# Optimization experiments

Hardware: AMD Instinct MI355X
Metric: run time of the kernel (lower is better)

The kernel has to match this reference:

```python
import jax, jax.numpy as jnp
import numpy as np

N = 50000   # nodes
E = 800000  # edges (before self-loops)
B = 256     # graphs in batch
F = 128     # input feature dim
H = 4       # heads per layer
C = 64      # out_channels per head
NEG_SLOPE = 0.2


def setup_inputs() -> dict:
    key = jax.random.key(0)
    ks = jax.random.split(key, 16)
    s = 0.05
    inp = {
        "x": jax.random.normal(ks[0], (N, F), dtype=jnp.float32),
        "edge_index": jax.random.randint(ks[1], (2, E), 0, N, dtype=jnp.int32),
        "batch": jnp.sort(jax.random.randint(ks[2], (N,), 0, B, dtype=jnp.int32)),
        # layer 1: F -> H*C
        "W1": jax.random.normal(ks[3], (F, H * C), dtype=jnp.float32) * s,
        "as1": jax.random.normal(ks[4], (H, C), dtype=jnp.float32) * s,
        "ad1": jax.random.normal(ks[5], (H, C), dtype=jnp.float32) * s,
        "b1": jnp.zeros((H * C,), dtype=jnp.float32),
        # layer 2: H*C -> H*C
        "W2": jax.random.normal(ks[6], (H * C, H * C), dtype=jnp.float32) * s,
        "as2": jax.random.normal(ks[7], (H, C), dtype=jnp.float32) * s,
        "ad2": jax.random.normal(ks[8], (H, C), dtype=jnp.float32) * s,
        "b2": jnp.zeros((H * C,), dtype=jnp.float32),
        # layer 3: H*C -> H*C
        "W3": jax.random.normal(ks[9], (H * C, H * C), dtype=jnp.float32) * s,
        "as3": jax.random.normal(ks[10], (H, C), dtype=jnp.float32) * s,
        "ad3": jax.random.normal(ks[11], (H, C), dtype=jnp.float32) * s,
        "b3": jnp.zeros((H * C,), dtype=jnp.float32),
    }
    return inp


def _gat_layer(x, src, dst, W, a_src, a_dst, bias):
    """PyG GATConv (concat=True, self-loops already included in src/dst)."""
    n = x.shape[0]
    xh = (x @ W).reshape(n, H, C)                      # [N,H,C]
    alpha_s = jnp.sum(xh * a_src, axis=-1)             # [N,H]
    alpha_d = jnp.sum(xh * a_dst, axis=-1)             # [N,H]
    logits = alpha_s[src] + alpha_d[dst]               # [E',H]
    logits = jnp.where(logits > 0, logits, NEG_SLOPE * logits)  # LeakyReLU
    # segment-wise softmax over destination neighborhoods
    m = jax.lax.stop_gradient(jax.ops.segment_max(logits, dst, num_segments=n))
    e = jnp.exp(logits - m[dst])
    z = jax.ops.segment_sum(e, dst, num_segments=n)
    alpha = e / (z[dst] + 1e-16)                       # [E',H]
    msg = xh[src] * alpha[:, :, None]                  # [E',H,C]
    out = jax.ops.segment_sum(msg, dst, num_segments=n)  # [N,H,C]
    return out.reshape(n, H * C) + bias


def reference(x, edge_index, batch, W1, as1, ad1, b1, W2, as2, ad2, b2, W3, as3, ad3, b3):
    n = x.shape[0]
    loops = jnp.arange(n, dtype=edge_index.dtype)
    src = jnp.concatenate([edge_index[0], loops])
    dst = jnp.concatenate([edge_index[1], loops])
    # dropout is identity at inference; activation = ReLU between layers
    h = jax.nn.relu(_gat_layer(x, src, dst, W1, as1, ad1, b1))
    h = jax.nn.relu(_gat_layer(h, src, dst, W2, as2, ad2, b2))
    h = _gat_layer(h, src, dst, W3, as3, ad3, b3)
    pooled = jax.ops.segment_max(h, batch, num_segments=B)  # global max pool -> [B, H*C]
    return jnp.squeeze(pooled)
```

## Files before the change

kernel.cpp:

```cpp
#include <hip/hip_runtime.h>
#include <hip/hip_fp16.h>
#include <math.h>

#define NN 50000
#define NE 800000
#define NT 850000
#define NB 256
#define FIN 128
#define HC 256
#define NH 4
#define CD 64
#define NEG 0.2f
#define SCAN_B 196
#define PSPL 8

typedef _Float16 half8 __attribute__((ext_vector_type(8)));
typedef float f32x4 __attribute__((ext_vector_type(4)));

__device__ __forceinline__ void gld16(const void* g, void* l) {
    __builtin_amdgcn_global_load_lds(
        (const __attribute__((address_space(1))) void*)g,
        (__attribute__((address_space(3))) void*)l, 16, 0, 0);
}


__global__ void zero_int_kernel(int* __restrict__ p, int n) {
    int i = blockIdx.x * blockDim.x + threadIdx.x;
    if (i < n) p[i] = 0;
}

__global__ void hist_kernel(const int* __restrict__ ei, int* __restrict__ cnt) {
    int e = blockIdx.x * blockDim.x + threadIdx.x;
    if (e < NE) {
        atomicAdd(&cnt[ei[NE + e]], 1);
    } else if (e < NT) {
        atomicAdd(&cnt[e - NE], 1);
    }
}

__global__ __launch_bounds__(256) void part_kernel(const int* __restrict__ cnt,
                                                   int* __restrict__ part) {
    __shared__ int red[4];
    int i = blockIdx.x * 256 + threadIdx.x;
    int v = (i < NN) ? cnt[i] : 0;
#pragma unroll
    for (int off = 32; off > 0; off >>= 1) v += __shfl_down(v, off);
    if ((threadIdx.x & 63) == 0) red[threadIdx.x >> 6] = v;
    __syncthreads();
    if (threadIdx.x == 0) part[blockIdx.x] = red[0] + red[1] + red[2] + red[3];
}

__global__ __launch_bounds__(256) void offs_kernel(const int* __restrict__ part,
                                                   int* __restrict__ boff) {
    __shared__ int sh[256];
    int t = threadIdx.x;
    sh[t] = (t < SCAN_B) ? part[t] : 0;
    __syncthreads();
    for (int off = 1; off < 256; off <<= 1) {
        int add = (t >= off) ? sh[t - off] : 0;
        __syncthreads();
        sh[t] += add;
        __syncthreads();
    }
    boff[t] = (t == 0) ? 0 : sh[t - 1];
}

__global__ __launch_bounds__(256) void write_scan_kernel(const int* __restrict__ cnt,
        const int* __restrict__ boff, int* __restrict__ rowptr, int* __restrict__ cursor) {
    __shared__ int sh[256];
    int t = threadIdx.x;
    int i = blockIdx.x * 256 + t;
    int v = (i < NN) ? cnt[i] : 0;
    sh[t] = v;
    __syncthreads();
    for (int off = 1; off < 256; off <<= 1) {
        int add = (t >= off) ? sh[t - off] : 0;
        __syncthreads();
        sh[t] += add;
        __syncthreads();
    }
    int run = boff[blockIdx.x] + sh[t] - v;
    if (i < NN) { rowptr[i] = run; cursor[i] = run; }
    if (i == NN - 1) rowptr[NN] = run + v;
}

__global__ void scatter_kernel(const int* __restrict__ ei, int* __restrict__ cursor,
                               int* __restrict__ colsrc) {
    int e = blockIdx.x * blockDim.x + threadIdx.x;
    int s, d;
    if (e < NE)      { s = ei[e]; d = ei[NE + e]; }
    else if (e < NT) { s = e - NE; d = s; }
    else return;
    int pos = atomicAdd(&cursor[d], 1);
    colsrc[pos] = s;
}

__global__ void batch_bounds_kernel(const int* __restrict__ batch, int* __restrict__ bstart) {
    int i = blockIdx.x * blockDim.x + threadIdx.x;
    if (i >= NN) return;
    int b = batch[i];
    if (i == 0) {
        for (int bb = 0; bb <= b; ++bb) bstart[bb] = 0;
    } else {
        int pb = batch[i - 1];
        if (pb != b) for (int bb = pb + 1; bb <= b; ++bb) bstart[bb] = i;
    }
    if (i == NN - 1) {
        for (int bb = b + 1; bb <= NB; ++bb) bstart[bb] = NN;
    }
}


template<int K>
__global__ __launch_bounds__(256) void wprep_kernel(const float* __restrict__ W,
                                                    _Float16* __restrict__ WtS) {
    __shared__ float sm[8][257];
    const int t = threadIdx.x;
    const int kb = blockIdx.x * 8;
#pragma unroll
    for (int i = 0; i < 8; ++i) {
        int idx = i * 256 + t;
        sm[idx >> 8][idx & 255] = W[(size_t)(kb + (idx >> 8)) * HC + (idx & 255)];
    }
    __syncthreads();
    half8 o;
#pragma unroll
    for (int r = 0; r < 8; ++r) o[r] = (_Float16)sm[r][t];
    *reinterpret_cast<half8*>(&WtS[((size_t)blockIdx.x * 256 + t) * 8]) = o;
}


template<int K, bool F32IN>
__global__ __launch_bounds__(256) void mfma_gemm_kernel(
        const _Float16* __restrict__ Xh, const _Float16* __restrict__ Xl,
        const float* __restrict__ Xf,
        const _Float16* __restrict__ WtS, __half* __restrict__ XHo,
        const float* __restrict__ as_g, const float* __restrict__ ad_g,
        float* __restrict__ aS, float* __restrict__ aD) {
    constexpr int C2 = 2 * K;
    constexpr int NSTEP = C2 / 32;
    constexpr int SPP = K / 32;
    __shared__ __align__(16) _Float16 As[4][64 * 32];
    __shared__ __align__(16) _Float16 Bs[4][32 * 128];
    const int t = threadIdx.x;
    const int lane = t & 63;
    const int wid = t >> 6;
    const int wm = wid & 1, wn = wid >> 1;
    const int cbb = blockIdx.x & 1;
    const int r0 = (blockIdx.x >> 1) * 64;
    const int cb0 = cbb * 128;
    const int l15 = lane & 15;
    const int kcl = lane >> 4;
    const int srowA = t >> 2;
    const int skcA  = t & 3;
    const int arow = min(r0 + srowA, NN - 1);

    f32x4 acc[2][4];
#pragma unroll
    for (int i = 0; i < 2; ++i)
#pragma unroll
        for (int j = 0; j < 4; ++j) acc[i][j] = (f32x4)0.f;

    float4 rA[3][2];

    auto loadA = [&](int s, float4& v0, float4& v1) {
        const int cbase = (s % SPP) * 32;
        if constexpr (F32IN) {
            const float* p = Xf + (size_t)arow * K + cbase + skcA * 8;
            v0 = *reinterpret_cast<const float4*>(p);
            v1 = *reinterpret_cast<const float4*>(p + 4);
        } else {
            const _Float16* src = (s < SPP) ? Xh : Xl;
            v0 = *reinterpret_cast<const float4*>(src + (size_t)arow * K + cbase + skcA * 8);
        }
    };
    auto writeA = [&](int s, int buf, float4 v0, float4 v1) {
        _Float16* d = &As[buf][(skcA * 64 + (srowA ^ skcA)) * 8];
        if constexpr (F32IN) {
            float f[8];
            *reinterpret_cast<float4*>(f) = v0;
            *reinterpret_cast<float4*>(f + 4) = v1;
            half8 h;
#pragma unroll
            for (int e = 0; e < 8; ++e) {
                _Float16 a = (_Float16)f[e];
                h[e] = (s >= SPP) ? (_Float16)(f[e] - (float)a) : a;
            }
            *reinterpret_cast<half8*>(d) = h;
        } else {
            *reinterpret_cast<float4*>(d) = v0;
        }
    };
    auto issueB = [&](int s, int buf) {
        const int kbase = (s % SPP) * 4;
#pragma unroll
        for (int r2 = 0; r2 < 2; ++r2) {
            int kc = r2 * 2 + (t >> 7);
            int col = t & 127;
            gld16(WtS + ((size_t)(kbase + kc) * 256 + cb0 + col) * 8,
                  &Bs[buf][(kc * 128 + col) * 8]);
        }
    };
    auto mfma_step = [&](int s, int buf) {
        half8 a0 = *reinterpret_cast<const half8*>(
            &As[buf][(kcl * 64 + ((wm * 32      + l15) ^ kcl)) * 8]);
        half8 a1 = *reinterpret_cast<const half8*>(
            &As[buf][(kcl * 64 + ((wm * 32 + 16 + l15) ^ kcl)) * 8]);
        const _Float16* bp = &Bs[buf][(kcl * 128 + wn * 64 + l15) * 8];
        __builtin_amdgcn_s_setprio(1);
#pragma unroll
        for (int nf = 0; nf < 4; ++nf) {
            half8 b = *reinterpret_cast<const half8*>(bp + nf * 16 * 8);
            acc[0][nf] = __builtin_amdgcn_mfma_f32_16x16x32_f16(a0, b, acc[0][nf], 0, 0, 0);
            acc[1][nf] = __builtin_amdgcn_mfma_f32_16x16x32_f16(a1, b, acc[1][nf], 0, 0, 0);
        }
        __builtin_amdgcn_s_setprio(0);
    };
    auto wait_steady = [&]() {
        if constexpr (F32IN) asm volatile("s_waitcnt vmcnt(8) lgkmcnt(0)" ::: "memory");
        else                 asm volatile("s_waitcnt vmcnt(6) lgkmcnt(0)" ::: "memory");
        __builtin_amdgcn_s_barrier();
        __builtin_amdgcn_sched_barrier(0);
    };

    loadA(0, rA[0][0], rA[0][1]); issueB(0, 0);
    loadA(1, rA[1][0], rA[1][1]); issueB(1, 1);
    loadA(2, rA[2][0], rA[2][1]); issueB(2, 2);
    writeA(0, 0, rA[0][0], rA[0][1]);
    wait_steady();

#pragma unroll
    for (int s = 0; s < NSTEP - 3; ++s) {
        loadA(s + 3, rA[(s + 3) % 3][0], rA[(s + 3) % 3][1]);
        issueB(s + 3, (s + 3) & 3);
        mfma_step(s, s & 3);
        writeA(s + 1, (s + 1) & 3, rA[(s + 1) % 3][0], rA[(s + 1) % 3][1]);
        wait_steady();
    }
    mfma_step(NSTEP - 3, (NSTEP - 3) & 3);
    writeA(NSTEP - 2, (NSTEP - 2) & 3, rA[(NSTEP - 2) % 3][0], rA[(NSTEP - 2) % 3][1]);
    if constexpr (F32IN) asm volatile("s_waitcnt vmcnt(4) lgkmcnt(0)" ::: "memory");
    else                 asm volatile("s_waitcnt vmcnt(3) lgkmcnt(0)" ::: "memory");
    __builtin_amdgcn_s_barrier();
    __builtin_amdgcn_sched_barrier(0);
    mfma_step(NSTEP - 2, (NSTEP - 2) & 3);
    writeA(NSTEP - 1, (NSTEP - 1) & 3, rA[(NSTEP - 1) % 3][0], rA[(NSTEP - 1) % 3][1]);
    asm volatile("s_waitcnt vmcnt(0) lgkmcnt(0)" ::: "memory");
    __builtin_amdgcn_s_barrier();
    __builtin_amdgcn_sched_barrier(0);
    mfma_step(NSTEP - 1, (NSTEP - 1) & 3);

    const int rb = r0 + wm * 32 + (lane >> 4) * 4;
    const int cbg = cb0 + wn * 64 + l15;
    const int head = cbb * 2 + wn;
    float asv[4], adv[4];
#pragma unroll
    for (int nf = 0; nf < 4; ++nf) {
        asv[nf] = as_g[cbg + nf * 16];
        adv[nf] = ad_g[cbg + nf * 16];
    }
#pragma unroll
    for (int mf = 0; mf < 2; ++mf)
#pragma unroll
        for (int r = 0; r < 4; ++r) {
            int row = rb + mf * 16 + r;
            float s0 = 0.f, d0 = 0.f;
#pragma unroll
            for (int nf = 0; nf < 4; ++nf) {
                float a = acc[mf][nf][r];
                s0 += a * asv[nf];
                d0 += a * adv[nf];
            }
#pragma unroll
            for (int off = 1; off < 16; off <<= 1) {
                s0 += __shfl_xor(s0, off);
                d0 += __shfl_xor(d0, off);
            }
            if (row < NN) {
                if (l15 == 0) {
                    aS[row * 4 + head] = s0;
                    aD[row * 4 + head] = d0;
                }
#pragma unroll
                for (int nf = 0; nf < 4; ++nf)
                    XHo[(size_t)row * HC + cbg + nf * 16] = __float2half(acc[mf][nf][r]);
            }
        }
}


#define LEAKY(v) ((v) > 0.f ? (v) : NEG * (v))

template<int RELU, int SPLIT>
__global__ __launch_bounds__(256) void aggregate_kernel(
        const int* __restrict__ rowptr, const int* __restrict__ colsrc,
        const float* __restrict__ aS, const float* __restrict__ aD,
        const __half* __restrict__ XH,
        const float* __restrict__ bias, float* __restrict__ OUT,
        __half* __restrict__ OUTh, __half* __restrict__ OUTl) {
    __shared__ float4 wbuf[4][64];
    __shared__ int    ibuf[4][64];
    const int wslot = threadIdx.x >> 6;
    int n = blockIdx.x * 4 + wslot;
    int lane = threadIdx.x & 63;
    bool lo = lane < 32;
    const __half2* xbase = reinterpret_cast<const __half2*>(XH);
    float4 adv = *reinterpret_cast<const float4*>(aD + n * 4);
    float zl = 0.f, zh = 0.f;
    float al0 = 0.f, al1 = 0.f, ah0 = 0.f, ah1 = 0.f;
    int jb = rowptr[n], je = rowptr[n + 1];
    for (int c0 = jb; c0 < je; c0 += 64) {
        int cnt = min(64, je - c0);
        {
            int e = min(c0 + lane, je - 1);
            int s = colsrc[e];
            float4 sv = *reinterpret_cast<const float4*>(aS + s * 4);
            float4 w;
            w.x = __expf(LEAKY(sv.x + adv.x));
            w.y = __expf(LEAKY(sv.y + adv.y));
            w.z = __expf(LEAKY(sv.z + adv.z));
            w.w = __expf(LEAKY(sv.w + adv.w));
            wbuf[wslot][lane] = w;
            ibuf[wslot][lane] = s;
        }
        int u = 0;
        for (; u + 8 <= cnt; u += 8) {
            int sidx[8];
            float4 w[8];
#pragma unroll
            for (int k = 0; k < 8; ++k) { sidx[k] = ibuf[wslot][u + k]; w[k] = wbuf[wslot][u + k]; }
            __half2 p[8], q[8];
#pragma unroll
            for (int k = 0; k < 8; ++k) {
                const __half2* xp = xbase + (size_t)sidx[k] * (HC / 2) + lane;
                p[k] = xp[0];
                q[k] = xp[64];
            }
#pragma unroll
            for (int k = 0; k < 8; ++k) {
                float wl = lo ? w[k].x : w[k].y, wh = lo ? w[k].z : w[k].w;
                float2 f = __half22float2(p[k]);
                al0 += wl * f.x; al1 += wl * f.y;
                f = __half22float2(q[k]);
                ah0 += wh * f.x; ah1 += wh * f.y;
                zl += wl; zh += wh;
            }
        }
        for (; u < cnt; ++u) {
            int s0 = ibuf[wslot][u];
            float4 w0 = wbuf[wslot][u];
            const __half2* xp = xbase + (size_t)s0 * (HC / 2) + lane;
            __half2 p0 = xp[0], q0 = xp[64];
            float w0l = lo ? w0.x : w0.y, w0h = lo ? w0.z : w0.w;
            float2 f = __half22float2(p0);
            al0 += w0l * f.x; al1 += w0l * f.y;
            f = __half22float2(q0);
            ah0 += w0h * f.x; ah1 += w0h * f.y;
            zl += w0l; zh += w0h;
        }
    }
    float izl = 1.f / (zl + 1e-16f), izh = 1.f / (zh + 1e-16f);
    float2 bl = reinterpret_cast<const float2*>(bias)[lane];
    float2 bh = reinterpret_cast<const float2*>(bias + 128)[lane];
    float o0 = al0 * izl + bl.x;
    float o1 = al1 * izl + bl.y;
    float o2 = ah0 * izh + bh.x;
    float o3 = ah1 * izh + bh.y;
    if (RELU) {
        o0 = fmaxf(o0, 0.f); o1 = fmaxf(o1, 0.f);
        o2 = fmaxf(o2, 0.f); o3 = fmaxf(o3, 0.f);
    }
    if (SPLIT) {
        __half h0 = __float2half(o0), h1 = __float2half(o1);
        __half h2 = __float2half(o2), h3 = __float2half(o3);
        __half2* ph = reinterpret_cast<__half2*>(OUTh + (size_t)n * HC) + lane;
        ph[0]  = __half2(h0, h1);
        ph[64] = __half2(h2, h3);
        __half2* pl = reinterpret_cast<__half2*>(OUTl + (size_t)n * HC) + lane;
        pl[0]  = __half2(__float2half(o0 - __half2float(h0)), __float2half(o1 - __half2float(h1)));
        pl[64] = __half2(__float2half(o2 - __half2float(h2)), __float2half(o3 - __half2float(h3)));
    } else {
        float2* op = reinterpret_cast<float2*>(OUT + (size_t)n * HC) + lane;
        op[0]  = make_float2(o0, o1);
        op[64] = make_float2(o2, o3);
    }
}


__global__ __launch_bounds__(256) void pool1_kernel(const float* __restrict__ Hf,
        const int* __restrict__ bstart, float* __restrict__ part) {
    int b = blockIdx.x / PSPL, sp = blockIdx.x % PSPL;
    int c = threadIdx.x;
    int i0 = bstart[b], i1 = bstart[b + 1];
    float m = -INFINITY;
    for (int i = i0 + sp; i < i1; i += PSPL) m = fmaxf(m, Hf[(size_t)i * HC + c]);
    part[(size_t)blockIdx.x * HC + c] = m;
}

__global__ __launch_bounds__(256) void pool2_kernel(const float* __restrict__ part,
        float* __restrict__ out) {
    int b = blockIdx.x;
    int c = threadIdx.x;
    float m = -INFINITY;
#pragma unroll
    for (int sp = 0; sp < PSPL; ++sp)
        m = fmaxf(m, part[(size_t)(b * PSPL + sp) * HC + c]);
    out[b * HC + c] = m;
}


extern "C" void kernel_launch(void* const* d_in, const int* in_sizes, int n_in,
                              void* d_out, int out_size, void* d_ws, size_t ws_size,
                              hipStream_t stream) {
    const float* x     = (const float*)d_in[0];
    const int*   ei    = (const int*)d_in[1];
    const int*   batch = (const int*)d_in[2];
    const float* W1  = (const float*)d_in[3];
    const float* as1 = (const float*)d_in[4];
    const float* ad1 = (const float*)d_in[5];
    const float* b1  = (const float*)d_in[6];
    const float* W2  = (const float*)d_in[7];
    const float* as2 = (const float*)d_in[8];
    const float* ad2 = (const float*)d_in[9];
    const float* b2  = (const float*)d_in[10];
    const float* W3  = (const float*)d_in[11];
    const float* as3 = (const float*)d_in[12];
    const float* ad3 = (const float*)d_in[13];
    const float* b3  = (const float*)d_in[14];
    float* out = (float*)d_out;

    __half* Hh  = (__half*)d_ws;
    __half* Hl  = Hh + (size_t)NN * HC;
    __half* XHh = Hl + (size_t)NN * HC;
    float* bufB = (float*)Hh;
    _Float16* WtS = (_Float16*)(XHh + (size_t)NN * HC);
    float*  aS  = (float*)(WtS + 256 * 256);
    float*  aD  = aS + NN * NH;
    float*  ppart = aD + NN * NH;
    int* cnt    = (int*)(ppart + (size_t)NB * PSPL * HC);
    int* rowptr = cnt + NN;
    int* cursor = rowptr + (NN + 1);
    int* colsrc = cursor + NN;
    int* bstart = colsrc + NT;
    int* part   = bstart + (NB + 1);
    int* boff   = part + SCAN_B;

    zero_int_kernel<<<(NN + 255) / 256, 256, 0, stream>>>(cnt, NN);
    hist_kernel<<<(NT + 255) / 256, 256, 0, stream>>>(ei, cnt);
    part_kernel<<<SCAN_B, 256, 0, stream>>>(cnt, part);
    offs_kernel<<<1, 256, 0, stream>>>(part, boff);
    write_scan_kernel<<<SCAN_B, 256, 0, stream>>>(cnt, boff, rowptr, cursor);
    scatter_kernel<<<(NT + 255) / 256, 256, 0, stream>>>(ei, cursor, colsrc);
    batch_bounds_kernel<<<(NN + 255) / 256, 256, 0, stream>>>(batch, bstart);

    const int gemm_grid = 2 * ((NN + 63) / 64);
    const int node_grid = NN / 4;

    wprep_kernel<FIN><<<FIN / 8, 256, 0, stream>>>(W1, WtS);
    mfma_gemm_kernel<FIN, true><<<gemm_grid, 256, 0, stream>>>(
        nullptr, nullptr, x, WtS, XHh, as1, ad1, aS, aD);
    aggregate_kernel<1, 1><<<node_grid, 256, 0, stream>>>(rowptr, colsrc, aS, aD, XHh, b1,
                                                          nullptr, Hh, Hl);

    wprep_kernel<HC><<<HC / 8, 256, 0, stream>>>(W2, WtS);
    mfma_gemm_kernel<HC, false><<<gemm_grid, 256, 0, stream>>>(
        (_Float16*)Hh, (_Float16*)Hl, nullptr, WtS, XHh, as2, ad2, aS, aD);
    aggregate_kernel<1, 1><<<node_grid, 256, 0, stream>>>(rowptr, colsrc, aS, aD, XHh, b2,
                                                          nullptr, Hh, Hl);

    wprep_kernel<HC><<<HC / 8, 256, 0, stream>>>(W3, WtS);
    mfma_gemm_kernel<HC, false><<<gemm_grid, 256, 0, stream>>>(
        (_Float16*)Hh, (_Float16*)Hl, nullptr, WtS, XHh, as3, ad3, aS, aD);
    aggregate_kernel<0, 0><<<node_grid, 256, 0, stream>>>(rowptr, colsrc, aS, aD, XHh, b3,
                                                          bufB, nullptr, nullptr);

    pool1_kernel<<<NB * PSPL, 256, 0, stream>>>(bufB, bstart, ppart);
    pool2_kernel<<<NB, 256, 0, stream>>>(ppart, out);
}
```

Before: 442.6 us.

## Drop hi/lo fp16 split in GEMM inputs and merge setup kernels

```diff
diff --git a/kernel.cpp b/kernel.cpp
--- a/kernel.cpp
+++ b/kernel.cpp
@@ -24,9 +24,21 @@
 }
 
 
-__global__ void zero_int_kernel(int* __restrict__ p, int n) {
-    int i = blockIdx.x * blockDim.x + threadIdx.x;
-    if (i < n) p[i] = 0;
+__global__ __launch_bounds__(256) void init_kernel(const int* __restrict__ batch,
+        int* __restrict__ cnt, int* __restrict__ bstart) {
+    int i = blockIdx.x * 256 + threadIdx.x;
+    if (i >= NN) return;
+    cnt[i] = 0;
+    int b = batch[i];
+    if (i == 0) {
+        for (int bb = 0; bb <= b; ++bb) bstart[bb] = 0;
+    } else {
+        int pb = batch[i - 1];
+        if (pb != b) for (int bb = pb + 1; bb <= b; ++bb) bstart[bb] = i;
+    }
+    if (i == NN - 1) {
+        for (int bb = b + 1; bb <= NB; ++bb) bstart[bb] = NN;
+    }
 }
 
 __global__ void hist_kernel(const int* __restrict__ ei, int* __restrict__ cnt) {
@@ -95,28 +107,22 @@
     colsrc[pos] = s;
 }
 
-__global__ void batch_bounds_kernel(const int* __restrict__ batch, int* __restrict__ bstart) {
-    int i = blockIdx.x * blockDim.x + threadIdx.x;
-    if (i >= NN) return;
-    int b = batch[i];
-    if (i == 0) {
-        for (int bb = 0; bb <= b; ++bb) bstart[bb] = 0;
-    } else {
-        int pb = batch[i - 1];
-        if (pb != b) for (int bb = pb + 1; bb <= b; ++bb) bstart[bb] = i;
-    }
-    if (i == NN - 1) {
-        for (int bb = b + 1; bb <= NB; ++bb) bstart[bb] = NN;
-    }
-}
-
-
-template<int K>
-__global__ __launch_bounds__(256) void wprep_kernel(const float* __restrict__ W,
-                                                    _Float16* __restrict__ WtS) {
+
+__global__ __launch_bounds__(256) void wprep_all_kernel(
+        const float* __restrict__ W1, const float* __restrict__ W2,
+        const float* __restrict__ W3,
+        _Float16* __restrict__ WtS1, _Float16* __restrict__ WtS2,
+        _Float16* __restrict__ WtS3) {
     __shared__ float sm[8][257];
     const int t = threadIdx.x;
-    const int kb = blockIdx.x * 8;
+    int b = blockIdx.x;
+    const float* W;
+    _Float16* O;
+    int lb;
+    if (b < 16)      { W = W1; O = WtS1; lb = b; }
+    else if (b < 48) { W = W2; O = WtS2; lb = b - 16; }
+    else             { W = W3; O = WtS3; lb = b - 48; }
+    const int kb = lb * 8;
 #pragma unroll
     for (int i = 0; i < 8; ++i) {
         int idx = i * 256 + t;
@@ -126,20 +132,17 @@
     half8 o;
 #pragma unroll
     for (int r = 0; r < 8; ++r) o[r] = (_Float16)sm[r][t];
-    *reinterpret_cast<half8*>(&WtS[((size_t)blockIdx.x * 256 + t) * 8]) = o;
+    *reinterpret_cast<half8*>(&O[((size_t)lb * 256 + t) * 8]) = o;
 }
 
 
 template<int K, bool F32IN>
 __global__ __launch_bounds__(256) void mfma_gemm_kernel(
-        const _Float16* __restrict__ Xh, const _Float16* __restrict__ Xl,
-        const float* __restrict__ Xf,
+        const _Float16* __restrict__ Xh, const float* __restrict__ Xf,
         const _Float16* __restrict__ WtS, __half* __restrict__ XHo,
         const float* __restrict__ as_g, const float* __restrict__ ad_g,
         float* __restrict__ aS, float* __restrict__ aD) {
-    constexpr int C2 = 2 * K;
-    constexpr int NSTEP = C2 / 32;
-    constexpr int SPP = K / 32;
+    constexpr int NSTEP = K / 32;
     __shared__ __align__(16) _Float16 As[4][64 * 32];
     __shared__ __align__(16) _Float16 Bs[4][32 * 128];
     const int t = threadIdx.x;
@@ -164,17 +167,16 @@
     float4 rA[3][2];
 
     auto loadA = [&](int s, float4& v0, float4& v1) {
-        const int cbase = (s % SPP) * 32;
+        const int cbase = s * 32;
         if constexpr (F32IN) {
             const float* p = Xf + (size_t)arow * K + cbase + skcA * 8;
             v0 = *reinterpret_cast<const float4*>(p);
             v1 = *reinterpret_cast<const float4*>(p + 4);
         } else {
-            const _Float16* src = (s < SPP) ? Xh : Xl;
-            v0 = *reinterpret_cast<const float4*>(src + (size_t)arow * K + cbase + skcA * 8);
+            v0 = *reinterpret_cast<const float4*>(Xh + (size_t)arow * K + cbase + skcA * 8);
         }
     };
-    auto writeA = [&](int s, int buf, float4 v0, float4 v1) {
+    auto writeA = [&](int buf, float4 v0, float4 v1) {
         _Float16* d = &As[buf][(skcA * 64 + (srowA ^ skcA)) * 8];
         if constexpr (F32IN) {
             float f[8];
@@ -182,17 +184,14 @@
             *reinterpret_cast<float4*>(f + 4) = v1;
             half8 h;
 #pragma unroll
-            for (int e = 0; e < 8; ++e) {
-                _Float16 a = (_Float16)f[e];
-                h[e] = (s >= SPP) ? (_Float16)(f[e] - (float)a) : a;
-            }
+            for (int e = 0; e < 8; ++e) h[e] = (_Float16)f[e];
             *reinterpret_cast<half8*>(d) = h;
         } else {
             *reinterpret_cast<float4*>(d) = v0;
         }
     };
     auto issueB = [&](int s, int buf) {
-        const int kbase = (s % SPP) * 4;
+        const int kbase = s * 4;
 #pragma unroll
         for (int r2 = 0; r2 < 2; ++r2) {
             int kc = r2 * 2 + (t >> 7);
@@ -201,7 +200,7 @@
                   &Bs[buf][(kc * 128 + col) * 8]);
         }
     };
-    auto mfma_step = [&](int s, int buf) {
+    auto mfma_step = [&](int buf) {
         half8 a0 = *reinterpret_cast<const half8*>(
             &As[buf][(kcl * 64 + ((wm * 32      + l15) ^ kcl)) * 8]);
         half8 a1 = *reinterpret_cast<const half8*>(
@@ -226,29 +225,29 @@
     loadA(0, rA[0][0], rA[0][1]); issueB(0, 0);
     loadA(1, rA[1][0], rA[1][1]); issueB(1, 1);
     loadA(2, rA[2][0], rA[2][1]); issueB(2, 2);
-    writeA(0, 0, rA[0][0], rA[0][1]);
+    writeA(0, rA[0][0], rA[0][1]);
     wait_steady();
 
 #pragma unroll
     for (int s = 0; s < NSTEP - 3; ++s) {
         loadA(s + 3, rA[(s + 3) % 3][0], rA[(s + 3) % 3][1]);
         issueB(s + 3, (s + 3) & 3);
-        mfma_step(s, s & 3);
-        writeA(s + 1, (s + 1) & 3, rA[(s + 1) % 3][0], rA[(s + 1) % 3][1]);
+        mfma_step(s & 3);
+        writeA((s + 1) & 3, rA[(s + 1) % 3][0], rA[(s + 1) % 3][1]);
         wait_steady();
     }
-    mfma_step(NSTEP - 3, (NSTEP - 3) & 3);
-    writeA(NSTEP - 2, (NSTEP - 2) & 3, rA[(NSTEP - 2) % 3][0], rA[(NSTEP - 2) % 3][1]);
+    mfma_step((NSTEP - 3) & 3);
+    writeA((NSTEP - 2) & 3, rA[(NSTEP - 2) % 3][0], rA[(NSTEP - 2) % 3][1]);
     if constexpr (F32IN) asm volatile("s_waitcnt vmcnt(4) lgkmcnt(0)" ::: "memory");
     else                 asm volatile("s_waitcnt vmcnt(3) lgkmcnt(0)" ::: "memory");
     __builtin_amdgcn_s_barrier();
     __builtin_amdgcn_sched_barrier(0);
-    mfma_step(NSTEP - 2, (NSTEP - 2) & 3);
-    writeA(NSTEP - 1, (NSTEP - 1) & 3, rA[(NSTEP - 1) % 3][0], rA[(NSTEP - 1) % 3][1]);
+    mfma_step((NSTEP - 2) & 3);
+    writeA((NSTEP - 1) & 3, rA[(NSTEP - 1) % 3][0], rA[(NSTEP - 1) % 3][1]);
     asm volatile("s_waitcnt vmcnt(0) lgkmcnt(0)" ::: "memory");
     __builtin_amdgcn_s_barrier();
     __builtin_amdgcn_sched_barrier(0);
-    mfma_step(NSTEP - 1, (NSTEP - 1) & 3);
+    mfma_step((NSTEP - 1) & 3);
 
     const int rb = r0 + wm * 32 + (lane >> 4) * 4;
     const int cbg = cb0 + wn * 64 + l15;
@@ -297,7 +296,7 @@
         const float* __restrict__ aS, const float* __restrict__ aD,
         const __half* __restrict__ XH,
         const float* __restrict__ bias, float* __restrict__ OUT,
-        __half* __restrict__ OUTh, __half* __restrict__ OUTl) {
+        __half* __restrict__ OUTh) {
     __shared__ float4 wbuf[4][64];
     __shared__ int    ibuf[4][64];
     const int wslot = threadIdx.x >> 6;
@@ -371,14 +370,9 @@
         o2 = fmaxf(o2, 0.f); o3 = fmaxf(o3, 0.f);
     }
     if (SPLIT) {
-        __half h0 = __float2half(o0), h1 = __float2half(o1);
-        __half h2 = __float2half(o2), h3 = __float2half(o3);
         __half2* ph = reinterpret_cast<__half2*>(OUTh + (size_t)n * HC) + lane;
-        ph[0]  = __half2(h0, h1);
-        ph[64] = __half2(h2, h3);
-        __half2* pl = reinterpret_cast<__half2*>(OUTl + (size_t)n * HC) + lane;
-        pl[0]  = __half2(__float2half(o0 - __half2float(h0)), __float2half(o1 - __half2float(h1)));
-        pl[64] = __half2(__float2half(o2 - __half2float(h2)), __float2half(o3 - __half2float(h3)));
+        ph[0]  = __half2(__float2half(o0), __float2half(o1));
+        ph[64] = __half2(__float2half(o2), __float2half(o3));
     } else {
         float2* op = reinterpret_cast<float2*>(OUT + (size_t)n * HC) + lane;
         op[0]  = make_float2(o0, o1);
@@ -430,11 +424,12 @@
     float* out = (float*)d_out;
 
     __half* Hh  = (__half*)d_ws;
-    __half* Hl  = Hh + (size_t)NN * HC;
-    __half* XHh = Hl + (size_t)NN * HC;
     float* bufB = (float*)Hh;
-    _Float16* WtS = (_Float16*)(XHh + (size_t)NN * HC);
-    float*  aS  = (float*)(WtS + 256 * 256);
+    __half* XHh = Hh + 2 * (size_t)NN * HC;
+    _Float16* WtS1 = (_Float16*)(XHh + (size_t)NN * HC);
+    _Float16* WtS2 = WtS1 + 16 * 256 * 8;
+    _Float16* WtS3 = WtS2 + 32 * 256 * 8;
+    float*  aS  = (float*)(WtS3 + 32 * 256 * 8);
     float*  aD  = aS + NN * NH;
     float*  ppart = aD + NN * NH;
     int* cnt    = (int*)(ppart + (size_t)NB * PSPL * HC);
@@ -445,34 +440,31 @@
     int* part   = bstart + (NB + 1);
     int* boff   = part + SCAN_B;
 
-    zero_int_kernel<<<(NN + 255) / 256, 256, 0, stream>>>(cnt, NN);
+    init_kernel<<<SCAN_B, 256, 0, stream>>>(batch, cnt, bstart);
     hist_kernel<<<(NT + 255) / 256, 256, 0, stream>>>(ei, cnt);
     part_kernel<<<SCAN_B, 256, 0, stream>>>(cnt, part);
     offs_kernel<<<1, 256, 0, stream>>>(part, boff);
     write_scan_kernel<<<SCAN_B, 256, 0, stream>>>(cnt, boff, rowptr, cursor);
     scatter_kernel<<<(NT + 255) / 256, 256, 0, stream>>>(ei, cursor, colsrc);
-    batch_bounds_kernel<<<(NN + 255) / 256, 256, 0, stream>>>(batch, bstart);
+    wprep_all_kernel<<<80, 256, 0, stream>>>(W1, W2, W3, WtS1, WtS2, WtS3);
 
     const int gemm_grid = 2 * ((NN + 63) / 64);
     const int node_grid = NN / 4;
 
-    wprep_kernel<FIN><<<FIN / 8, 256, 0, stream>>>(W1, WtS);
     mfma_gemm_kernel<FIN, true><<<gemm_grid, 256, 0, stream>>>(
-        nullptr, nullptr, x, WtS, XHh, as1, ad1, aS, aD);
+        nullptr, x, WtS1, XHh, as1, ad1, aS, aD);
     aggregate_kernel<1, 1><<<node_grid, 256, 0, stream>>>(rowptr, colsrc, aS, aD, XHh, b1,
-                                                          nullptr, Hh, Hl);
-
-    wprep_kernel<HC><<<HC / 8, 256, 0, stream>>>(W2, WtS);
+                                                          nullptr, Hh);
+
     mfma_gemm_kernel<HC, false><<<gemm_grid, 256, 0, stream>>>(
-        (_Float16*)Hh, (_Float16*)Hl, nullptr, WtS, XHh, as2, ad2, aS, aD);
+        (_Float16*)Hh, nullptr, WtS2, XHh, as2, ad2, aS, aD);
     aggregate_kernel<1, 1><<<node_grid, 256, 0, stream>>>(rowptr, colsrc, aS, aD, XHh, b2,
-                                                          nullptr, Hh, Hl);
-
-    wprep_kernel<HC><<<HC / 8, 256, 0, stream>>>(W3, WtS);
+                                                          nullptr, Hh);
+
     mfma_gemm_kernel<HC, false><<<gemm_grid, 256, 0, stream>>>(
-        (_Float16*)Hh, (_Float16*)Hl, nullptr, WtS, XHh, as3, ad3, aS, aD);
+        (_Float16*)Hh, nullptr, WtS3, XHh, as3, ad3, aS, aD);
     aggregate_kernel<0, 0><<<node_grid, 256, 0, stream>>>(rowptr, colsrc, aS, aD, XHh, b3,
-                                                          bufB, nullptr, nullptr);
+                                                          bufB, nullptr);
 
     pool1_kernel<<<NB * PSPL, 256, 0, stream>>>(bufB, bstart, ppart);
     pool2_kernel<<<NB, 256, 0, stream>>>(ppart, out);
```

Measured after the change: 397.5 us. -10.2%, faster.
